# Kernel optimization log

Hardware: AMD Instinct MI355X
Metric: run time of the kernel (lower is better)

The kernel has to match this reference:

```python
import math
import jax, jax.numpy as jnp
import numpy as np


def setup_inputs() -> dict:
    B, MA, ME = 512, 64, 256
    d_model, d_qk, N = 256, 32, 200000
    rng = np.random.default_rng(0)
    actor_len = rng.integers(1, MA + 1, B)
    actee_len = rng.integers(1, ME + 1, B)
    # flat scatter positions: indices(1) + indices(0) * max_len
    qindices = np.concatenate([np.arange(l) + i * MA for i, l in enumerate(actor_len)]).astype(np.int64)
    kindices = np.concatenate([np.arange(l) + i * ME for i, l in enumerate(actee_len)]).astype(np.int64)
    A, E = len(qindices), len(kindices)
    actors = rng.integers(0, N, A)            # absolute indices into x (offsets pre-applied)
    actees = rng.integers(0, N, E)
    # previous action for each actor must index a valid actee of its env
    prev_actions = rng.integers(0, np.repeat(actee_len, actor_len))
    key = jax.random.key(0)
    k0, k1, k2 = jax.random.split(key, 3)
    s = 1.0 / math.sqrt(d_model)
    return {
        "x": jax.random.normal(k0, (N, d_model), jnp.float32),
        "Wq": jax.random.normal(k1, (d_model, d_qk), jnp.float32) * s,
        "bq": jnp.zeros((d_qk,), jnp.float32),
        "Wk": jax.random.normal(k2, (d_model, d_qk), jnp.float32) * s,
        "bk": jnp.zeros((d_qk,), jnp.float32),
        "actors": jnp.asarray(actors, jnp.int32),
        "qindices": jnp.asarray(qindices, jnp.int32),
        "actees": jnp.asarray(actees, jnp.int32),
        "kindices": jnp.asarray(kindices, jnp.int32),
        "prev_actions": jnp.asarray(prev_actions, jnp.int32),
        "B": B, "max_actors": MA, "max_actees": ME,
    }


def reference(x, Wq, bq, Wk, bk, actors, qindices, actees, kindices, prev_actions, B, max_actors, max_actees):
    d_qk = Wq.shape[1]
    scale = 1.0 / math.sqrt(d_qk)
    queries = x[actors] @ Wq + bq                         # [A, d_qk] ragged gather + project
    keys = x[actees] @ Wk + bk                            # [E, d_qk]
    # scatter into zero-padded (queries) / one-padded (keys) buffers
    pq = jnp.zeros((B * max_actors, d_qk), x.dtype).at[qindices].set(queries).reshape(B, max_actors, d_qk)
    qmask = jnp.zeros((B * max_actors,), x.dtype).at[qindices].set(1.0).reshape(B, max_actors)
    pk = jnp.ones((B * max_actees, d_qk), x.dtype).at[kindices].set(keys).reshape(B, max_actees, d_qk)
    kmask = jnp.zeros((B * max_actees,), x.dtype).at[kindices].set(1.0).reshape(B, max_actees)
    logits = jnp.einsum("bqd,bkd->bqk", pq, pk) * scale   # [B, max_actors, max_actees]
    valid = qmask[:, :, None] * kmask[:, None, :]
    logits = jnp.where(valid == 0, jnp.asarray(-1e9, x.dtype), logits)
    # prev_actions branch: scatter actions into one-padded buffer
    padded_actions = jnp.ones((B * max_actors,), jnp.int32).at[qindices].set(prev_actions).reshape(B, max_actors)
    logp = jax.nn.log_softmax(logits, axis=-1)
    logprob = jnp.take_along_axis(logp, padded_actions[:, :, None], axis=-1)[..., 0]  # [B, max_actors]
    entropy = -jnp.sum(jnp.exp(logp) * logp, axis=-1)
    # gather-back to ragged layout
    return (
        padded_actions.reshape(-1)[qindices],
        logprob.reshape(-1)[qindices],
        entropy.reshape(-1)[qindices],
        logits,
    )
```

## Files before the change

### kernel.cpp

```cpp
#include <hip/hip_runtime.h>
#include <math.h>

#define MA 64
#define ME 256
#define DM 256
#define DQK 32
#define ENVSTRIDE (MA * ME)
#define MASKVAL -998244352.0f
#define QK_SCALE 0.17677669529663687f
#define KSTR 40

typedef __attribute__((ext_vector_type(8))) short bf16x8;
typedef __attribute__((ext_vector_type(4))) float f32x4;
typedef unsigned short u16;

__device__ __forceinline__ int lb(const int* __restrict__ a, int n, int v){
  int lo = 0, hi = n;
  while (lo < hi){ int mid = (lo + hi) >> 1; if (a[mid] < v) lo = mid + 1; else hi = mid; }
  return lo;
}
__device__ __forceinline__ unsigned pk2bf(float lo, float hi){
  unsigned ul = __float_as_uint(lo); ul = ul + 0x7FFFu + ((ul >> 16) & 1u);
  unsigned uh = __float_as_uint(hi); uh = uh + 0x7FFFu + ((uh >> 16) & 1u);
  return (ul >> 16) | (uh & 0xFFFF0000u);
}
__device__ __forceinline__ u16 f2bu(float f){
  unsigned u = __float_as_uint(f);
  return (u16)((u + 0x7FFFu + ((u >> 16) & 1u)) >> 16);
}

__global__ __launch_bounds__(256)
void fused_env(const float* __restrict__ x,  const float* __restrict__ Wq, const float* __restrict__ bq,
               const float* __restrict__ Wk, const float* __restrict__ bk,
               const int* __restrict__ actors, const int* __restrict__ qindices,
               const int* __restrict__ actees, const int* __restrict__ kindices,
               const int* __restrict__ prev_actions, int A, int E, float* __restrict__ out)
{
  __shared__ __align__(16) unsigned wfr32[2 * 8 * 2 * 256];
  __shared__ u16 kb[ME * KSTR];
  __shared__ u16 qsm[MA * KSTR];
  __shared__ int srange[4];

  const int t = threadIdx.x, b = blockIdx.x;
  if (t < 4) {
    const int* arr = (t < 2) ? qindices : kindices;
    const int nn = (t < 2) ? A : E;
    const int vv = (t == 0) ? b * MA : (t == 1) ? (b + 1) * MA
                 : (t == 2) ? b * ME : (b + 1) * ME;
    srange[t] = lb(arr, nn, vv);
  }

  #pragma unroll
  for (int ii = 0; ii < 32; ++ii) {
    const int i = t + ii * 256;
    const int p = i & 3, ln = (i >> 2) & 63, nt = (i >> 8) & 1, kk = (i >> 9) & 7, wh = i >> 12;
    const int k0  = kk * 32 + (ln >> 4) * 8 + 2 * p;
    const int col = nt * 16 + (ln & 15);
    const float* W = wh ? Wq : Wk;
    wfr32[i] = pk2bf(W[(size_t)k0 * DQK + col], W[(size_t)(k0 + 1) * DQK + col]);
  }
  __syncthreads();

  const int qstart = srange[0], qlen = srange[1] - srange[0];
  const int kstart = srange[2], klen = srange[3] - srange[2];

  const int lane = t & 63, w = t >> 6;
  const int lr = lane & 15, lq = lane >> 4;

  const float bkv0 = bk[lr], bkv1 = bk[16 + lr];
  const float bqv0 = bq[lr], bqv1 = bq[16 + lr];

  const int kt = (klen + 15) >> 4;
  const int qt = (qlen + 15) >> 4;
  const int ntiles = kt + qt;

  for (int i = w; i < ntiles; i += 4) {
    const bool isk = (i < kt);
    const int  rbase = isk ? (i << 4) : ((i - kt) << 4);
    const int  len   = isk ? klen : qlen;
    const int  start = isk ? kstart : qstart;
    const int* gath  = isk ? actees : actors;
    u16*       dst   = isk ? kb : qsm;
    const unsigned* fbase = &wfr32[(isk ? 0 : 4096) + lane * 4];

    const int arow = start + min(rbase + lr, len - 1);
    const float* xr = x + (size_t)gath[arow] * DM + lq * 8;

    float4 cx[16];
    #pragma unroll
    for (int kk = 0; kk < 8; ++kk) {
      cx[2*kk]   = *(const float4*)(xr + kk * 32);
      cx[2*kk+1] = *(const float4*)(xr + kk * 32 + 4);
    }

    const float v0 = isk ? bkv0 : bqv0, v1 = isk ? bkv1 : bqv1;
    f32x4 a0 = {v0, v0, v0, v0}, a1 = {v1, v1, v1, v1};
    #pragma unroll
    for (int kk = 0; kk < 8; ++kk) {
      union { unsigned u[4]; bf16x8 v; } fa;
      fa.u[0] = pk2bf(cx[2*kk].x,   cx[2*kk].y);
      fa.u[1] = pk2bf(cx[2*kk].z,   cx[2*kk].w);
      fa.u[2] = pk2bf(cx[2*kk+1].x, cx[2*kk+1].y);
      fa.u[3] = pk2bf(cx[2*kk+1].z, cx[2*kk+1].w);
      const bf16x8 b0 = *(const bf16x8*)(fbase + kk * 512);
      const bf16x8 b1 = *(const bf16x8*)(fbase + kk * 512 + 256);
      a0 = __builtin_amdgcn_mfma_f32_16x16x32_bf16(fa.v, b0, a0, 0, 0, 0);
      a1 = __builtin_amdgcn_mfma_f32_16x16x32_bf16(fa.v, b1, a1, 0, 0, 0);
    }
    #pragma unroll
    for (int reg = 0; reg < 4; ++reg) {
      const int row = rbase + 4 * lq + reg;
      if (row < len) {
        dst[row * KSTR + lr]      = f2bu(a0[reg]);
        dst[row * KSTR + 16 + lr] = f2bu(a1[reg]);
      }
    }
  }
  __syncthreads();

  float* out_lg = out + (size_t)3 * A + (size_t)b * ENVSTRIDE;
  const int row0 = 16 * w;

  if (row0 >= qlen) {
    const float4 mv = make_float4(MASKVAL, MASKVAL, MASKVAL, MASKVAL);
    float4* o4 = (float4*)out_lg;
    #pragma unroll
    for (int rr = 0; rr < 16; ++rr) o4[(row0 + rr) * 64 + lane] = mv;
    return;
  }

  const bf16x8 afr = *(const bf16x8*)&qsm[(row0 + lr) * KSTR + lq * 8];
  f32x4 acc[16];
  #pragma unroll
  for (int nt = 0; nt < 16; ++nt) {
    const bf16x8 bfr2 = *(const bf16x8*)&kb[(16 * nt + lr) * KSTR + lq * 8];
    f32x4 z = {0.f, 0.f, 0.f, 0.f};
    acc[nt] = __builtin_amdgcn_mfma_f32_16x16x32_bf16(afr, bfr2, z, 0, 0, 0);
  }

  int par[4];
  float m[4], spa[4], es[4], ts[4];
  #pragma unroll
  for (int reg = 0; reg < 4; ++reg) {
    const int r = row0 + 4 * lq + reg;
    par[reg] = (r < qlen) ? (prev_actions[qstart + r] & (ME - 1)) : -1;
    m[reg] = MASKVAL; spa[reg] = MASKVAL; es[reg] = 0.f; ts[reg] = 0.f;
  }

  #pragma unroll
  for (int nt = 0; nt < 16; ++nt) {
    const int col = 16 * nt + lr;
    const bool kv = (col < klen);
    #pragma unroll
    for (int reg = 0; reg < 4; ++reg) {
      const float d = kv ? acc[nt][reg] * QK_SCALE : MASKVAL;
      acc[nt][reg] = d;
      m[reg] = fmaxf(m[reg], d);
      if (col == par[reg]) spa[reg] = d;
    }
  }
  #pragma unroll
  for (int off = 1; off < 16; off <<= 1) {
    #pragma unroll
    for (int reg = 0; reg < 4; ++reg) {
      m[reg]   = fmaxf(m[reg],   __shfl_xor(m[reg],   off));
      spa[reg] = fmaxf(spa[reg], __shfl_xor(spa[reg], off));
    }
  }
  #pragma unroll
  for (int nt = 0; nt < 16; ++nt) {
    #pragma unroll
    for (int reg = 0; reg < 4; ++reg) {
      const float dd = acc[nt][reg] - m[reg];
      if (dd > -80.f) { const float e = __expf(dd); es[reg] += e; ts[reg] += e * dd; }
    }
  }
  #pragma unroll
  for (int off = 1; off < 16; off <<= 1) {
    #pragma unroll
    for (int reg = 0; reg < 4; ++reg) {
      es[reg] += __shfl_xor(es[reg], off);
      ts[reg] += __shfl_xor(ts[reg], off);
    }
  }

  #pragma unroll
  for (int nt = 0; nt < 16; ++nt) {
    #pragma unroll
    for (int reg = 0; reg < 4; ++reg) {
      const int r = row0 + 4 * lq + reg;
      out_lg[r * ME + 16 * nt + lr] = (r < qlen) ? acc[nt][reg] : MASKVAL;
    }
  }
  if (lr == 0) {
    #pragma unroll
    for (int reg = 0; reg < 4; ++reg) {
      const int r = row0 + 4 * lq + reg;
      if (r < qlen) {
        const float lS = __logf(fmaxf(es[reg], 1e-30f));
        out[qstart + r]         = (float)par[reg];
        out[A + qstart + r]     = spa[reg] - m[reg] - lS;
        out[2 * A + qstart + r] = lS - ts[reg] / es[reg];
      }
    }
  }
}

extern "C" void kernel_launch(void* const* d_in, const int* in_sizes, int n_in,
                              void* d_out, int out_size, void* d_ws, size_t ws_size,
                              hipStream_t stream) {
  const float* x  = (const float*)d_in[0];
  const float* Wq = (const float*)d_in[1];
  const float* bq = (const float*)d_in[2];
  const float* Wk = (const float*)d_in[3];
  const float* bk = (const float*)d_in[4];
  const int* actors       = (const int*)d_in[5];
  const int* qindices     = (const int*)d_in[6];
  const int* actees       = (const int*)d_in[7];
  const int* kindices     = (const int*)d_in[8];
  const int* prev_actions = (const int*)d_in[9];

  const int A = in_sizes[5];
  const int E = in_sizes[7];
  const int B = (out_size - 3 * A) / ENVSTRIDE;
  if (B <= 0) return;

  fused_env<<<dim3(B), dim3(256), 0, stream>>>(
      x, Wq, bq, Wk, bk, actors, qindices, actees, kindices, prev_actions,
      A, E, (float*)d_out);
}
```

Before: 41.06 us.

## Split fused kernel into weight-pack, global projection and per-env logits kernels

Replaces the single per-env kernel with three launches. One block packs Wq/Wk into bf16 MFMA fragments once, instead of every block repacking them. A grid-wide projection kernel then assigns one 16-row tile to each wave across all actors and actees, so uneven env sizes no longer unbalance the projection work. It scatters the bf16 projections into a staging area that reuses each env's own logits output region, and the logits kernel reads that staging into shared memory before overwriting it. The cost is two extra launches and a global memory round trip for the projections, and it relies on the staging layout lining up with the output buffer.

After: 45.20 us. 1.1x slower.

```diff
diff --git a/kernel.cpp b/kernel.cpp
--- a/kernel.cpp
+++ b/kernel.cpp
@@ -9,6 +9,7 @@
 #define MASKVAL -998244352.0f
 #define QK_SCALE 0.17677669529663687f
 #define KSTR 40
+#define ESTR16 32768
 
 typedef __attribute__((ext_vector_type(8))) short bf16x8;
 typedef __attribute__((ext_vector_type(4))) float f32x4;
@@ -30,13 +31,90 @@
 }
 
 __global__ __launch_bounds__(256)
-void fused_env(const float* __restrict__ x,  const float* __restrict__ Wq, const float* __restrict__ bq,
-               const float* __restrict__ Wk, const float* __restrict__ bk,
+void pack_w(const float* __restrict__ Wk, const float* __restrict__ Wq,
+            unsigned* __restrict__ wfr_g){
+  const int t = threadIdx.x;
+  #pragma unroll
+  for (int ii = 0; ii < 32; ++ii) {
+    const int i = t + ii * 256;
+    const int p = i & 3, ln = (i >> 2) & 63, nt = (i >> 8) & 1, kk = (i >> 9) & 7, wh = i >> 12;
+    const int k0  = kk * 32 + (ln >> 4) * 8 + 2 * p;
+    const int col = nt * 16 + (ln & 15);
+    const float* W = wh ? Wq : Wk;
+    wfr_g[i] = pk2bf(W[(size_t)k0 * DQK + col], W[(size_t)(k0 + 1) * DQK + col]);
+  }
+}
+
+__global__ __launch_bounds__(256)
+void proj_mfma(const float* __restrict__ x,
+               const float* __restrict__ bq, const float* __restrict__ bk,
                const int* __restrict__ actors, const int* __restrict__ qindices,
                const int* __restrict__ actees, const int* __restrict__ kindices,
-               const int* __restrict__ prev_actions, int A, int E, float* __restrict__ out)
+               int A, int E, int nKt, int nTot,
+               const unsigned* __restrict__ wfr_g, u16* __restrict__ stage)
 {
-  __shared__ __align__(16) unsigned wfr32[2 * 8 * 2 * 256];
+  const int lane = threadIdx.x & 63, w = threadIdx.x >> 6;
+  const int wid = blockIdx.x * 4 + w;
+  if (wid >= nTot) return;
+
+  const bool isk  = (wid < nKt);
+  const int  tile = isk ? wid : wid - nKt;
+  const int  n    = isk ? E : A;
+  const int  rbase = tile << 4;
+  const int  lr = lane & 15, lq = lane >> 4;
+
+  const int arow = min(rbase + lr, n - 1);
+  const int src  = isk ? actees[arow] : actors[arow];
+  const float* xr = x + (size_t)src * DM + lq * 8;
+
+  const unsigned* fb = wfr_g + (isk ? 0 : 4096) + lane * 4;
+  bf16x8 bfr[8][2];
+  #pragma unroll
+  for (int kk = 0; kk < 8; ++kk) {
+    bfr[kk][0] = *(const bf16x8*)(fb + kk * 512);
+    bfr[kk][1] = *(const bf16x8*)(fb + kk * 512 + 256);
+  }
+  const float* bb = isk ? bk : bq;
+  const float bv0 = bb[lr], bv1 = bb[16 + lr];
+
+  float4 cx[16];
+  #pragma unroll
+  for (int kk = 0; kk < 8; ++kk) {
+    cx[2*kk]   = *(const float4*)(xr + kk * 32);
+    cx[2*kk+1] = *(const float4*)(xr + kk * 32 + 4);
+  }
+
+  f32x4 a0 = {bv0, bv0, bv0, bv0}, a1 = {bv1, bv1, bv1, bv1};
+  #pragma unroll
+  for (int kk = 0; kk < 8; ++kk) {
+    union { unsigned u[4]; bf16x8 v; } fa;
+    fa.u[0] = pk2bf(cx[2*kk].x,   cx[2*kk].y);
+    fa.u[1] = pk2bf(cx[2*kk].z,   cx[2*kk].w);
+    fa.u[2] = pk2bf(cx[2*kk+1].x, cx[2*kk+1].y);
+    fa.u[3] = pk2bf(cx[2*kk+1].z, cx[2*kk+1].w);
+    a0 = __builtin_amdgcn_mfma_f32_16x16x32_bf16(fa.v, bfr[kk][0], a0, 0, 0, 0);
+    a1 = __builtin_amdgcn_mfma_f32_16x16x32_bf16(fa.v, bfr[kk][1], a1, 0, 0, 0);
+  }
+
+  #pragma unroll
+  for (int reg = 0; reg < 4; ++reg) {
+    const int row = rbase + 4 * lq + reg;
+    if (row < n) {
+      const int idx = isk ? kindices[row] : qindices[row];
+      const int env = isk ? (idx >> 8) : (idx >> 6);
+      const int pos = isk ? (idx & (ME - 1)) : (idx & (MA - 1));
+      u16* dst = stage + (size_t)env * ESTR16 + (isk ? 0 : 8192) + pos * 32;
+      dst[lr]      = f2bu(a0[reg]);
+      dst[16 + lr] = f2bu(a1[reg]);
+    }
+  }
+}
+
+__global__ __launch_bounds__(256)
+void logits_kernel(const int* __restrict__ qindices, const int* __restrict__ kindices,
+                   const int* __restrict__ prev_actions, const u16* __restrict__ stage,
+                   int A, int E, float* __restrict__ out)
+{
   __shared__ u16 kb[ME * KSTR];
   __shared__ u16 qsm[MA * KSTR];
   __shared__ int srange[4];
@@ -50,73 +128,25 @@
     srange[t] = lb(arr, nn, vv);
   }
 
-  #pragma unroll
-  for (int ii = 0; ii < 32; ++ii) {
-    const int i = t + ii * 256;
-    const int p = i & 3, ln = (i >> 2) & 63, nt = (i >> 8) & 1, kk = (i >> 9) & 7, wh = i >> 12;
-    const int k0  = kk * 32 + (ln >> 4) * 8 + 2 * p;
-    const int col = nt * 16 + (ln & 15);
-    const float* W = wh ? Wq : Wk;
-    wfr32[i] = pk2bf(W[(size_t)k0 * DQK + col], W[(size_t)(k0 + 1) * DQK + col]);
+  const u16* sk = stage + (size_t)b * ESTR16;
+  const u16* sq = sk + 8192;
+  #pragma unroll
+  for (int ii = 0; ii < 4; ++ii) {
+    const int i = t * 4 + ii;
+    const int row = i >> 2, c8 = (i & 3) * 8;
+    *(bf16x8*)&kb[row * KSTR + c8] = *(const bf16x8*)(sk + i * 8);
+  }
+  {
+    const int row = t >> 2, c8 = (t & 3) * 8;
+    *(bf16x8*)&qsm[row * KSTR + c8] = *(const bf16x8*)(sq + t * 8);
   }
   __syncthreads();
 
   const int qstart = srange[0], qlen = srange[1] - srange[0];
-  const int kstart = srange[2], klen = srange[3] - srange[2];
+  const int klen   = srange[3] - srange[2];
 
   const int lane = t & 63, w = t >> 6;
   const int lr = lane & 15, lq = lane >> 4;
-
-  const float bkv0 = bk[lr], bkv1 = bk[16 + lr];
-  const float bqv0 = bq[lr], bqv1 = bq[16 + lr];
-
-  const int kt = (klen + 15) >> 4;
-  const int qt = (qlen + 15) >> 4;
-  const int ntiles = kt + qt;
-
-  for (int i = w; i < ntiles; i += 4) {
-    const bool isk = (i < kt);
-    const int  rbase = isk ? (i << 4) : ((i - kt) << 4);
-    const int  len   = isk ? klen : qlen;
-    const int  start = isk ? kstart : qstart;
-    const int* gath  = isk ? actees : actors;
-    u16*       dst   = isk ? kb : qsm;
-    const unsigned* fbase = &wfr32[(isk ? 0 : 4096) + lane * 4];
-
-    const int arow = start + min(rbase + lr, len - 1);
-    const float* xr = x + (size_t)gath[arow] * DM + lq * 8;
-
-    float4 cx[16];
-    #pragma unroll
-    for (int kk = 0; kk < 8; ++kk) {
-      cx[2*kk]   = *(const float4*)(xr + kk * 32);
-      cx[2*kk+1] = *(const float4*)(xr + kk * 32 + 4);
-    }
-
-    const float v0 = isk ? bkv0 : bqv0, v1 = isk ? bkv1 : bqv1;
-    f32x4 a0 = {v0, v0, v0, v0}, a1 = {v1, v1, v1, v1};
-    #pragma unroll
-    for (int kk = 0; kk < 8; ++kk) {
-      union { unsigned u[4]; bf16x8 v; } fa;
-      fa.u[0] = pk2bf(cx[2*kk].x,   cx[2*kk].y);
-      fa.u[1] = pk2bf(cx[2*kk].z,   cx[2*kk].w);
-      fa.u[2] = pk2bf(cx[2*kk+1].x, cx[2*kk+1].y);
-      fa.u[3] = pk2bf(cx[2*kk+1].z, cx[2*kk+1].w);
-      const bf16x8 b0 = *(const bf16x8*)(fbase + kk * 512);
-      const bf16x8 b1 = *(const bf16x8*)(fbase + kk * 512 + 256);
-      a0 = __builtin_amdgcn_mfma_f32_16x16x32_bf16(fa.v, b0, a0, 0, 0, 0);
-      a1 = __builtin_amdgcn_mfma_f32_16x16x32_bf16(fa.v, b1, a1, 0, 0, 0);
-    }
-    #pragma unroll
-    for (int reg = 0; reg < 4; ++reg) {
-      const int row = rbase + 4 * lq + reg;
-      if (row < len) {
-        dst[row * KSTR + lr]      = f2bu(a0[reg]);
-        dst[row * KSTR + 16 + lr] = f2bu(a1[reg]);
-      }
-    }
-  }
-  __syncthreads();
 
   float* out_lg = out + (size_t)3 * A + (size_t)b * ENVSTRIDE;
   const int row0 = 16 * w;
@@ -225,7 +255,17 @@
   const int B = (out_size - 3 * A) / ENVSTRIDE;
   if (B <= 0) return;
 
-  fused_env<<<dim3(B), dim3(256), 0, stream>>>(
-      x, Wq, bq, Wk, bk, actors, qindices, actees, kindices, prev_actions,
-      A, E, (float*)d_out);
-}
+  float* out = (float*)d_out;
+  u16* stage = (u16*)(out + (((size_t)3 * A + 3) & ~(size_t)3));
+  unsigned* wfr_g = (unsigned*)(stage + 16384);
+
+  const int nKt = (E + 15) / 16;
+  const int nQt = (A + 15) / 16;
+  const int nTot = nKt + nQt;
+
+  pack_w<<<dim3(1), dim3(256), 0, stream>>>(Wk, Wq, wfr_g);
+  proj_mfma<<<dim3((nTot + 3) / 4), dim3(256), 0, stream>>>(
+      x, bq, bk, actors, qindices, actees, kindices, A, E, nKt, nTot, wfr_g, stage);
+  logits_kernel<<<dim3(B), dim3(256), 0, stream>>>(
+      qindices, kindices, prev_actions, stage, A, E, out);
+}
```

## Prepack weights once, double block width, split logits columns across wave pairs

Applied to the files above, without the earlier changes.

Weight packing to bf16 fragments moves out of every block into a separate one-block pre-kernel that writes to workspace, so the fused kernel reads the fragments from global/L2 instead of rebuilding them in LDS per block. The fused kernel now runs 512 threads (8 waves): projection tiles are spread over 8 waves, and each 16-row query tile's 256 logit columns are split between two waves. The two halves' softmax statistics (max, sum, entropy term, selected logit) are merged through shared memory with rescaling. This adds an extra kernel launch, a dependency between the two kernels, and an additional block barrier.

Measured after the change: 44.46 us. 1.08x slower.

```diff
diff --git a/kernel.cpp b/kernel.cpp
--- a/kernel.cpp
+++ b/kernel.cpp
@@ -30,26 +30,9 @@
 }
 
 __global__ __launch_bounds__(256)
-void fused_env(const float* __restrict__ x,  const float* __restrict__ Wq, const float* __restrict__ bq,
-               const float* __restrict__ Wk, const float* __restrict__ bk,
-               const int* __restrict__ actors, const int* __restrict__ qindices,
-               const int* __restrict__ actees, const int* __restrict__ kindices,
-               const int* __restrict__ prev_actions, int A, int E, float* __restrict__ out)
-{
-  __shared__ __align__(16) unsigned wfr32[2 * 8 * 2 * 256];
-  __shared__ u16 kb[ME * KSTR];
-  __shared__ u16 qsm[MA * KSTR];
-  __shared__ int srange[4];
-
-  const int t = threadIdx.x, b = blockIdx.x;
-  if (t < 4) {
-    const int* arr = (t < 2) ? qindices : kindices;
-    const int nn = (t < 2) ? A : E;
-    const int vv = (t == 0) ? b * MA : (t == 1) ? (b + 1) * MA
-                 : (t == 2) ? b * ME : (b + 1) * ME;
-    srange[t] = lb(arr, nn, vv);
-  }
-
+void pack_w(const float* __restrict__ Wk, const float* __restrict__ Wq,
+            unsigned* __restrict__ wfr_g){
+  const int t = threadIdx.x;
   #pragma unroll
   for (int ii = 0; ii < 32; ++ii) {
     const int i = t + ii * 256;
@@ -57,55 +40,80 @@
     const int k0  = kk * 32 + (ln >> 4) * 8 + 2 * p;
     const int col = nt * 16 + (ln & 15);
     const float* W = wh ? Wq : Wk;
-    wfr32[i] = pk2bf(W[(size_t)k0 * DQK + col], W[(size_t)(k0 + 1) * DQK + col]);
+    wfr_g[i] = pk2bf(W[(size_t)k0 * DQK + col], W[(size_t)(k0 + 1) * DQK + col]);
+  }
+}
+
+__global__ __launch_bounds__(512, 4)
+void fused_env(const float* __restrict__ x,
+               const float* __restrict__ bq, const float* __restrict__ bk,
+               const int* __restrict__ actors, const int* __restrict__ qindices,
+               const int* __restrict__ actees, const int* __restrict__ kindices,
+               const int* __restrict__ prev_actions,
+               const unsigned* __restrict__ wfr_g,
+               int A, int E, float* __restrict__ out)
+{
+  __shared__ u16 kb[ME * KSTR];
+  __shared__ u16 qsm[MA * KSTR];
+  __shared__ float red[8][16][4];
+  __shared__ int srange[4];
+
+  const int t = threadIdx.x, b = blockIdx.x;
+  const int lane = t & 63, w = t >> 6;
+  const int lr = lane & 15, lq = lane >> 4;
+
+  if (t < 4) {
+    const int* arr = (t < 2) ? qindices : kindices;
+    const int nn = (t < 2) ? A : E;
+    const int vv = (t == 0) ? b * MA : (t == 1) ? (b + 1) * MA
+                 : (t == 2) ? b * ME : (b + 1) * ME;
+    srange[t] = lb(arr, nn, vv);
   }
   __syncthreads();
-
   const int qstart = srange[0], qlen = srange[1] - srange[0];
   const int kstart = srange[2], klen = srange[3] - srange[2];
-
-  const int lane = t & 63, w = t >> 6;
-  const int lr = lane & 15, lq = lane >> 4;
-
-  const float bkv0 = bk[lr], bkv1 = bk[16 + lr];
-  const float bqv0 = bq[lr], bqv1 = bq[16 + lr];
 
   const int kt = (klen + 15) >> 4;
   const int qt = (qlen + 15) >> 4;
   const int ntiles = kt + qt;
 
-  for (int i = w; i < ntiles; i += 4) {
+  for (int i = w; i < ntiles; i += 8) {
     const bool isk = (i < kt);
     const int  rbase = isk ? (i << 4) : ((i - kt) << 4);
     const int  len   = isk ? klen : qlen;
     const int  start = isk ? kstart : qstart;
     const int* gath  = isk ? actees : actors;
     u16*       dst   = isk ? kb : qsm;
-    const unsigned* fbase = &wfr32[(isk ? 0 : 4096) + lane * 4];
+    const unsigned* fb = wfr_g + (isk ? 0 : 4096) + lane * 4;
 
     const int arow = start + min(rbase + lr, len - 1);
     const float* xr = x + (size_t)gath[arow] * DM + lq * 8;
 
-    float4 cx[16];
-    #pragma unroll
-    for (int kk = 0; kk < 8; ++kk) {
-      cx[2*kk]   = *(const float4*)(xr + kk * 32);
-      cx[2*kk+1] = *(const float4*)(xr + kk * 32 + 4);
-    }
-
-    const float v0 = isk ? bkv0 : bqv0, v1 = isk ? bkv1 : bqv1;
-    f32x4 a0 = {v0, v0, v0, v0}, a1 = {v1, v1, v1, v1};
-    #pragma unroll
-    for (int kk = 0; kk < 8; ++kk) {
-      union { unsigned u[4]; bf16x8 v; } fa;
-      fa.u[0] = pk2bf(cx[2*kk].x,   cx[2*kk].y);
-      fa.u[1] = pk2bf(cx[2*kk].z,   cx[2*kk].w);
-      fa.u[2] = pk2bf(cx[2*kk+1].x, cx[2*kk+1].y);
-      fa.u[3] = pk2bf(cx[2*kk+1].z, cx[2*kk+1].w);
-      const bf16x8 b0 = *(const bf16x8*)(fbase + kk * 512);
-      const bf16x8 b1 = *(const bf16x8*)(fbase + kk * 512 + 256);
-      a0 = __builtin_amdgcn_mfma_f32_16x16x32_bf16(fa.v, b0, a0, 0, 0, 0);
-      a1 = __builtin_amdgcn_mfma_f32_16x16x32_bf16(fa.v, b1, a1, 0, 0, 0);
+    const float* bb = isk ? bk : bq;
+    const float bv0 = bb[lr], bv1 = bb[16 + lr];
+    f32x4 a0 = {bv0, bv0, bv0, bv0}, a1 = {bv1, bv1, bv1, bv1};
+
+    #pragma unroll
+    for (int h = 0; h < 2; ++h) {
+      float4 cx[8];
+      #pragma unroll
+      for (int k2 = 0; k2 < 4; ++k2) {
+        cx[2*k2]   = *(const float4*)(xr + h * 128 + k2 * 32);
+        cx[2*k2+1] = *(const float4*)(xr + h * 128 + k2 * 32 + 4);
+      }
+      #pragma unroll
+      for (int k2 = 0; k2 < 4; ++k2) {
+        const int kk = h * 4 + k2;
+        union { unsigned u[4]; bf16x8 v; } fa;
+        fa.u[0] = pk2bf(cx[2*k2].x,   cx[2*k2].y);
+        fa.u[1] = pk2bf(cx[2*k2].z,   cx[2*k2].w);
+        fa.u[2] = pk2bf(cx[2*k2+1].x, cx[2*k2+1].y);
+        fa.u[3] = pk2bf(cx[2*k2+1].z, cx[2*k2+1].w);
+        const bf16x8 b0 = *(const bf16x8*)(fb + kk * 512);
+        const bf16x8 b1 = *(const bf16x8*)(fb + kk * 512 + 256);
+        a0 = __builtin_amdgcn_mfma_f32_16x16x32_bf16(fa.v, b0, a0, 0, 0, 0);
+        a1 = __builtin_amdgcn_mfma_f32_16x16x32_bf16(fa.v, b1, a1, 0, 0, 0);
+      }
     }
     #pragma unroll
     for (int reg = 0; reg < 4; ++reg) {
@@ -119,80 +127,112 @@
   __syncthreads();
 
   float* out_lg = out + (size_t)3 * A + (size_t)b * ENVSTRIDE;
-  const int row0 = 16 * w;
-
-  if (row0 >= qlen) {
+  const int tt = w >> 1, ch = w & 1;
+  const int row0 = 16 * tt;
+  const bool live = (row0 < qlen);
+
+  f32x4 acc[8];
+  int par[4];
+  float m[4], spa[4], es[4], ts[4];
+
+  if (live) {
+    const bf16x8 afr = *(const bf16x8*)&qsm[(row0 + lr) * KSTR + lq * 8];
+    #pragma unroll
+    for (int nt = 0; nt < 8; ++nt) {
+      const int ntg = 8 * ch + nt;
+      const bf16x8 bfr2 = *(const bf16x8*)&kb[(16 * ntg + lr) * KSTR + lq * 8];
+      f32x4 z = {0.f, 0.f, 0.f, 0.f};
+      acc[nt] = __builtin_amdgcn_mfma_f32_16x16x32_bf16(afr, bfr2, z, 0, 0, 0);
+    }
+    #pragma unroll
+    for (int reg = 0; reg < 4; ++reg) {
+      const int r = row0 + 4 * lq + reg;
+      par[reg] = (r < qlen) ? (prev_actions[qstart + r] & (ME - 1)) : -1;
+      m[reg] = MASKVAL; spa[reg] = MASKVAL; es[reg] = 0.f; ts[reg] = 0.f;
+    }
+    #pragma unroll
+    for (int nt = 0; nt < 8; ++nt) {
+      const int col = 128 * ch + 16 * nt + lr;
+      const bool kv = (col < klen);
+      #pragma unroll
+      for (int reg = 0; reg < 4; ++reg) {
+        const float d = kv ? acc[nt][reg] * QK_SCALE : MASKVAL;
+        acc[nt][reg] = d;
+        m[reg] = fmaxf(m[reg], d);
+        if (col == par[reg]) spa[reg] = d;
+      }
+    }
+    #pragma unroll
+    for (int off = 1; off < 16; off <<= 1) {
+      #pragma unroll
+      for (int reg = 0; reg < 4; ++reg) {
+        m[reg]   = fmaxf(m[reg],   __shfl_xor(m[reg],   off));
+        spa[reg] = fmaxf(spa[reg], __shfl_xor(spa[reg], off));
+      }
+    }
+    #pragma unroll
+    for (int nt = 0; nt < 8; ++nt) {
+      #pragma unroll
+      for (int reg = 0; reg < 4; ++reg) {
+        const float dd = acc[nt][reg] - m[reg];
+        if (dd > -80.f) { const float e = __expf(dd); es[reg] += e; ts[reg] += e * dd; }
+      }
+    }
+    #pragma unroll
+    for (int off = 1; off < 16; off <<= 1) {
+      #pragma unroll
+      for (int reg = 0; reg < 4; ++reg) {
+        es[reg] += __shfl_xor(es[reg], off);
+        ts[reg] += __shfl_xor(ts[reg], off);
+      }
+    }
+    if (lr == 0) {
+      #pragma unroll
+      for (int reg = 0; reg < 4; ++reg) {
+        const int ridx = 4 * lq + reg;
+        red[w][ridx][0] = m[reg];  red[w][ridx][1] = spa[reg];
+        red[w][ridx][2] = es[reg]; red[w][ridx][3] = ts[reg];
+      }
+    }
+  }
+  __syncthreads();
+
+  if (!live) {
     const float4 mv = make_float4(MASKVAL, MASKVAL, MASKVAL, MASKVAL);
     float4* o4 = (float4*)out_lg;
     #pragma unroll
-    for (int rr = 0; rr < 16; ++rr) o4[(row0 + rr) * 64 + lane] = mv;
+    for (int rr = 0; rr < 8; ++rr) {
+      const int r = row0 + 2 * rr + (lane >> 5);
+      o4[r * 64 + 32 * ch + (lane & 31)] = mv;
+    }
     return;
   }
 
-  const bf16x8 afr = *(const bf16x8*)&qsm[(row0 + lr) * KSTR + lq * 8];
-  f32x4 acc[16];
-  #pragma unroll
-  for (int nt = 0; nt < 16; ++nt) {
-    const bf16x8 bfr2 = *(const bf16x8*)&kb[(16 * nt + lr) * KSTR + lq * 8];
-    f32x4 z = {0.f, 0.f, 0.f, 0.f};
-    acc[nt] = __builtin_amdgcn_mfma_f32_16x16x32_bf16(afr, bfr2, z, 0, 0, 0);
-  }
-
-  int par[4];
-  float m[4], spa[4], es[4], ts[4];
+  const int other = w ^ 1;
   #pragma unroll
   for (int reg = 0; reg < 4; ++reg) {
-    const int r = row0 + 4 * lq + reg;
-    par[reg] = (r < qlen) ? (prev_actions[qstart + r] & (ME - 1)) : -1;
-    m[reg] = MASKVAL; spa[reg] = MASKVAL; es[reg] = 0.f; ts[reg] = 0.f;
+    const int ridx = 4 * lq + reg;
+    const float mb  = red[other][ridx][0];
+    const float spb = red[other][ridx][1];
+    const float eb  = red[other][ridx][2];
+    const float tb  = red[other][ridx][3];
+    const float M  = fmaxf(m[reg], mb);
+    const float sa = __expf(m[reg] - M), sb = __expf(mb - M);
+    ts[reg]  = (ts[reg] + es[reg] * (m[reg] - M)) * sa + (tb + eb * (mb - M)) * sb;
+    es[reg]  = es[reg] * sa + eb * sb;
+    m[reg]   = M;
+    spa[reg] = fmaxf(spa[reg], spb);
   }
 
   #pragma unroll
-  for (int nt = 0; nt < 16; ++nt) {
-    const int col = 16 * nt + lr;
-    const bool kv = (col < klen);
-    #pragma unroll
-    for (int reg = 0; reg < 4; ++reg) {
-      const float d = kv ? acc[nt][reg] * QK_SCALE : MASKVAL;
-      acc[nt][reg] = d;
-      m[reg] = fmaxf(m[reg], d);
-      if (col == par[reg]) spa[reg] = d;
-    }
-  }
-  #pragma unroll
-  for (int off = 1; off < 16; off <<= 1) {
-    #pragma unroll
-    for (int reg = 0; reg < 4; ++reg) {
-      m[reg]   = fmaxf(m[reg],   __shfl_xor(m[reg],   off));
-      spa[reg] = fmaxf(spa[reg], __shfl_xor(spa[reg], off));
-    }
-  }
-  #pragma unroll
-  for (int nt = 0; nt < 16; ++nt) {
-    #pragma unroll
-    for (int reg = 0; reg < 4; ++reg) {
-      const float dd = acc[nt][reg] - m[reg];
-      if (dd > -80.f) { const float e = __expf(dd); es[reg] += e; ts[reg] += e * dd; }
-    }
-  }
-  #pragma unroll
-  for (int off = 1; off < 16; off <<= 1) {
-    #pragma unroll
-    for (int reg = 0; reg < 4; ++reg) {
-      es[reg] += __shfl_xor(es[reg], off);
-      ts[reg] += __shfl_xor(ts[reg], off);
-    }
-  }
-
-  #pragma unroll
-  for (int nt = 0; nt < 16; ++nt) {
+  for (int nt = 0; nt < 8; ++nt) {
     #pragma unroll
     for (int reg = 0; reg < 4; ++reg) {
       const int r = row0 + 4 * lq + reg;
-      out_lg[r * ME + 16 * nt + lr] = (r < qlen) ? acc[nt][reg] : MASKVAL;
-    }
-  }
-  if (lr == 0) {
+      out_lg[r * ME + 128 * ch + 16 * nt + lr] = (r < qlen) ? acc[nt][reg] : MASKVAL;
+    }
+  }
+  if (ch == 0 && lr == 0) {
     #pragma unroll
     for (int reg = 0; reg < 4; ++reg) {
       const int r = row0 + 4 * lq + reg;
@@ -225,7 +265,10 @@
   const int B = (out_size - 3 * A) / ENVSTRIDE;
   if (B <= 0) return;
 
-  fused_env<<<dim3(B), dim3(256), 0, stream>>>(
-      x, Wq, bq, Wk, bk, actors, qindices, actees, kindices, prev_actions,
-      A, E, (float*)d_out);
-}
+  unsigned* wfr_g = (unsigned*)d_ws;
+
+  pack_w<<<dim3(1), dim3(256), 0, stream>>>(Wk, Wq, wfr_g);
+  fused_env<<<dim3(B), dim3(512), 0, stream>>>(
+      x, bq, bk, actors, qindices, actees, kindices, prev_actions,
+      wfr_g, A, E, (float*)d_out);
+}
```
